# Kernel tuning notes

Hardware: AMD Instinct MI355X
Metric: run time of the kernel (lower is better)

## Reference

```python
import jax, jax.numpy as jnp
import numpy as np

S, O, H = 8, 1024, 1024
B, N = 32, 512

def setup_inputs() -> dict:
    key = jax.random.key(0)
    k1, k2, k3, k4 = jax.random.split(key, 4)
    x = jax.random.normal(k1, (B, N, H), dtype=jnp.float32)
    subject_id = jax.random.randint(k2, (B,), 0, S)
    # kaiming_uniform_(a=sqrt(5)) on [S,O,H]: fan_in=H, gain=sqrt(2/(1+5)), bound=gain*sqrt(3/fan_in)
    wbound = jnp.sqrt(2.0 / 6.0) * jnp.sqrt(3.0 / H)
    weight = jax.random.uniform(k3, (S, O, H), minval=-wbound, maxval=wbound, dtype=jnp.float32)
    bbound = 1.0 / jnp.sqrt(H)
    bias = jax.random.uniform(k4, (S, O), minval=-bbound, maxval=bbound, dtype=jnp.float32)
    return {"x": x, "subject_id": subject_id, "weight": weight, "bias": bias}

def reference(x, subject_id, weight, bias):
    # Per-sample weight gather + batched matmul + bias add
    W = weight[subject_id]          # [B, O, H]
    b = bias[subject_id]            # [B, O]
    y = jnp.einsum('bnh,boh->bno', x, W) + b[:, None, :]
    return y
```

## Files before the change

kernel.cpp:

```cpp
#include <hip/hip_runtime.h>


constexpr int S_DIM = 8;
constexpr int O_DIM = 1024;
constexpr int H_DIM = 1024;
constexpr int B_DIM = 32;
constexpr int N_DIM = 512;

constexpr int BM = 256;
constexpr int BN = 256;
constexpr int BK = 64;
constexpr int NKT = H_DIM / BK;

constexpr long long X_ELEMS = (long long)B_DIM * N_DIM * H_DIM;
constexpr size_t XB_BYTES = (size_t)X_ELEMS * 2;

typedef short bf16x8 __attribute__((ext_vector_type(8)));
typedef float f32x4 __attribute__((ext_vector_type(4)));
typedef float f32x2 __attribute__((ext_vector_type(2)));
typedef __bf16 bf16x2 __attribute__((ext_vector_type(2)));

__device__ __forceinline__ unsigned int cvt_pk_bf16(float a, float b) {
  f32x2 v;
  v[0] = a;
  v[1] = b;
  bf16x2 r = __builtin_convertvector(v, bf16x2);
  return __builtin_bit_cast(unsigned int, r);
}

__device__ __forceinline__ void gload_lds16(const void* g, void* l) {
  __builtin_amdgcn_global_load_lds(
      (const __attribute__((address_space(1))) unsigned int*)g,
      (__attribute__((address_space(3))) unsigned int*)l, 16, 0, 0);
}

__global__ __launch_bounds__(256) void cvt_kernel(
    const float* __restrict__ x, const float* __restrict__ w,
    unsigned short* __restrict__ xb, unsigned short* __restrict__ wb) {
  const int blk = blockIdx.x;
  const float* src;
  unsigned short* dst;
  long long base;
  if (blk < 4096) {
    src = x; dst = xb; base = (long long)blk * 4096;
  } else {
    src = w; dst = wb; base = (long long)(blk - 4096) * 4096;
  }
  const long long e0 = base + threadIdx.x * 4;
#pragma unroll
  for (int c = 0; c < 4; ++c) {
    const f32x4 v = __builtin_nontemporal_load((const f32x4*)(src + e0 + c * 1024));
    uint2 u;
    u.x = cvt_pk_bf16(v[0], v[1]);
    u.y = cvt_pk_bf16(v[2], v[3]);
    *(uint2*)(dst + e0 + c * 1024) = u;
  }
}

#define BAR() __builtin_amdgcn_s_barrier()
#define SB0() __builtin_amdgcn_sched_barrier(0)
#define VMW(N) asm volatile("s_waitcnt vmcnt(" #N ")" ::: "memory")
#define LGKM0()                                            \
  do {                                                     \
    asm volatile("s_waitcnt lgkmcnt(0)" ::: "memory");     \
    __builtin_amdgcn_sched_barrier(0);                     \
  } while (0)

#define LDA4T(DST, ABUF, MB)                                             \
  do {                                                                   \
    _Pragma("unroll") for (int m_ = 0; m_ < 4; ++m_) {                   \
      const int ar_ = wr * 128 + ((MB) + m_) * 16 + lcol;                \
      const unsigned short* ap_ = (ABUF) + ar_ * BK;                     \
      DST[m_][0] = *(const bf16x8*)(ap_ + (pc0 << 3));                   \
      DST[m_][1] = *(const bf16x8*)(ap_ + ((pc0 ^ 4) << 3));             \
    }                                                                    \
  } while (0)

#define LDB2T(DST, BBUF, NB)                                             \
  do {                                                                   \
    _Pragma("unroll") for (int n_ = 0; n_ < 2; ++n_) {                   \
      const int br_ = wc * 64 + ((NB) + n_) * 16 + lcol;                 \
      const unsigned short* bp_ = (BBUF) + br_ * BK;                     \
      DST[n_][0] = *(const bf16x8*)(bp_ + (pc0 << 3));                   \
      DST[n_][1] = *(const bf16x8*)(bp_ + ((pc0 ^ 4) << 3));             \
    }                                                                    \
  } while (0)

#define MM4(AF, BF, MB, NB)                                                 \
  do {                                                                      \
    _Pragma("unroll") for (int m_ = 0; m_ < 4; ++m_)                        \
    _Pragma("unroll") for (int n_ = 0; n_ < 2; ++n_)                        \
    _Pragma("unroll") for (int x_ = 0; x_ < 2; ++x_)                        \
      acc[(MB) + m_][(NB) + n_] = __builtin_amdgcn_mfma_f32_16x16x32_bf16(  \
          AF[m_][x_], BF[n_][x_], acc[(MB) + m_][(NB) + n_], 0, 0, 0);      \
  } while (0)

#define STAGE_A(H, DST, KT)                                                 \
  do {                                                                      \
    gload_lds16(agA + (size_t)((H) * 64) * H_DIM + (KT) * 64,               \
                (DST) + ((H) * 64 + wid * 8) * BK);                         \
    gload_lds16(agA + (size_t)((H) * 64 + 128) * H_DIM + (KT) * 64,         \
                (DST) + ((H) * 64 + 128 + wid * 8) * BK);                   \
  } while (0)

#define STAGE_B(S, DST, KT)                                                 \
  do {                                                                      \
    gload_lds16(bgB0 + (size_t)((S) * 32) * H_DIM + (KT) * 64,              \
                (DST) + (bq0 + (S) * 32) * BK);                             \
    gload_lds16(bgB1 + (size_t)((S) * 32) * H_DIM + (KT) * 64,              \
                (DST) + (bq1 + (S) * 32) * BK);                             \
  } while (0)

#define KTILE(KT, AC, BC, AO, BO)                                        \
  do {                                                                   \
        \
    LGKM0();                                                             \
    __builtin_amdgcn_s_setprio(1);                                       \
    MM4(af, bfL, 0, 0);                                                  \
    __builtin_amdgcn_s_setprio(0);                                       \
    LDB2T(bfH, BC, 2);                             \
    if ((KT) + 1 < NKT) STAGE_A(1, AO, (KT) + 1);                        \
    SB0();                                                               \
    BAR();                                                               \
                                                  \
    LGKM0();                                                             \
    __builtin_amdgcn_s_setprio(1);                                       \
    MM4(af, bfH, 0, 2);                                                  \
    __builtin_amdgcn_s_setprio(0);                                       \
    LDA4T(af, AC, 4);                           \
    if ((KT) + 1 < NKT) STAGE_B(1, BO, (KT) + 1);                        \
    SB0();                                                               \
    BAR();                                                               \
                                                  \
    LGKM0();                                                             \
    __builtin_amdgcn_s_setprio(1);                                       \
    MM4(af, bfH, 4, 2);                                                  \
    __builtin_amdgcn_s_setprio(0);                                       \
    if ((KT) + 2 < NKT) {                                                \
      STAGE_A(0, AC, (KT) + 2);                                          \
      STAGE_B(0, BC, (KT) + 2);                                          \
      VMW(8);            \
    } else if ((KT) + 2 == NKT) {                                        \
      VMW(4);                                                            \
    }                                                                    \
    SB0();                                                               \
    BAR();                                                               \
                                                  \
    LGKM0();                                                             \
    __builtin_amdgcn_s_setprio(1);                                       \
    MM4(af, bfL, 4, 0);                                                  \
    __builtin_amdgcn_s_setprio(0);                                       \
    if ((KT) + 1 < NKT) {                                                \
      LDA4T(af, AO, 0);                                 \
      LDB2T(bfL, BO, 0);                                \
      if ((KT) + 2 < NKT) VMW(4);          \
      else VMW(0);                   \
    }                                                                    \
    SB0();                                                               \
    BAR();                                                               \
  } while (0)

__global__ __launch_bounds__(512, 2) void scl_gemm(
    const unsigned short* __restrict__ xb, const int* __restrict__ subject_id,
    const unsigned short* __restrict__ wb, const float* __restrict__ bias,
    float* __restrict__ out) {
  __shared__ __align__(16) unsigned short As[2][BM * BK];
  __shared__ __align__(16) unsigned short Bs[2][BN * BK];

  const int tid = threadIdx.x;
  const int lane = tid & 63;
  const int wid = tid >> 6;
  const int wr = wid >> 2;
  const int wc = wid & 3;
  const int lcol = lane & 15;
  const int lq = lane >> 4;
  const int rl = lane >> 3;
  const int pc0 = lq ^ (lane & 7);

  const int bid = blockIdx.x;
  const int b = (bid & 7) * 4 + ((bid >> 3) & 3);
  const int t = bid >> 5;
  const int n0 = (t & 1) * BM;
  const int o0 = (t >> 1) * BN;
  const int sid = subject_id[b];

  const int skc = ((lane & 7) ^ rl) << 3;
  const unsigned short* agA =
      xb + (size_t)(b * N_DIM + n0 + wid * 8 + rl) * H_DIM + skc;
  const int bq0 = ((wid * 2) >> 2) * 64 + ((wid * 2) & 3) * 8;
  const int bq1 = ((wid * 2 + 1) >> 2) * 64 + ((wid * 2 + 1) & 3) * 8;
  const unsigned short* bgB0 =
      wb + (size_t)(sid * O_DIM + o0 + bq0 + rl) * H_DIM + skc;
  const unsigned short* bgB1 =
      wb + (size_t)(sid * O_DIM + o0 + bq1 + rl) * H_DIM + skc;

  unsigned short* const As0 = &As[0][0];
  unsigned short* const As1 = &As[1][0];
  unsigned short* const Bs0 = &Bs[0][0];
  unsigned short* const Bs1 = &Bs[1][0];

  f32x4 acc[8][4];
#pragma unroll
  for (int mi = 0; mi < 8; ++mi)
#pragma unroll
    for (int ni = 0; ni < 4; ++ni) {
      f32x4 z = {0.f, 0.f, 0.f, 0.f};
      acc[mi][ni] = z;
    }

  bf16x8 af[4][2];
  bf16x8 bfL[2][2];
  bf16x8 bfH[2][2];

  STAGE_A(0, As0, 0);
  STAGE_B(0, Bs0, 0);
  STAGE_A(1, As0, 0);
  STAGE_B(1, Bs0, 0);
  STAGE_A(0, As1, 1);
  STAGE_B(0, Bs1, 1);
  VMW(4);
  BAR();
  LDA4T(af, As0, 0);
  LDB2T(bfL, Bs0, 0);
  SB0();

#pragma unroll 1
  for (int kt = 0; kt < NKT; kt += 2) {
    KTILE(kt, As0, Bs0, As1, Bs1);
    KTILE(kt + 1, As1, Bs1, As0, Bs0);
  }

  float bv[4];
#pragma unroll
  for (int ni = 0; ni < 4; ++ni)
    bv[ni] = bias[sid * O_DIM + o0 + wc * 64 + ni * 16 + lcol];

  float* outb =
      out + (size_t)(b * N_DIM + n0 + wr * 128) * O_DIM + o0 + wc * 64 + lcol;
#pragma unroll
  for (int mi = 0; mi < 8; ++mi) {
#pragma unroll
    for (int r = 0; r < 4; ++r) {
      float* orow = outb + (size_t)(mi * 16 + lq * 4 + r) * O_DIM;
#pragma unroll
      for (int ni = 0; ni < 4; ++ni)
        orow[ni * 16] = acc[mi][ni][r] + bv[ni];
    }
  }
}

extern "C" void kernel_launch(void* const* d_in, const int* in_sizes, int n_in,
                              void* d_out, int out_size, void* d_ws, size_t ws_size,
                              hipStream_t stream) {
  const float* x = (const float*)d_in[0];
  const int* subject_id = (const int*)d_in[1];
  const float* weight = (const float*)d_in[2];
  const float* bias = (const float*)d_in[3];
  float* out = (float*)d_out;

  unsigned short* xb = (unsigned short*)d_ws;
  unsigned short* wb = (unsigned short*)((char*)d_ws + XB_BYTES);

  cvt_kernel<<<6144, 256, 0, stream>>>(x, weight, xb, wb);

  scl_gemm<<<256, 512, 0, stream>>>(xb, subject_id, wb, bias, out);
}
```

Before: 177.6 us.

## Fuse fp32-to-bf16 conversion of x into GEMM LDS path with triple buffering

Removes the separate conversion pass over x: the GEMM now stages fp32 x tiles directly into LDS and converts them to bf16 while loading MFMA fragments. Only the weights still go through a standalone conversion kernel. To make room for fp32 A tiles, BK drops to 32 and the pipeline becomes a three-stage LDS ring with new swizzles and a two-phase k-tile schedule. This avoids writing and rereading a 32 MB bf16 copy of x, but it doubles A-side LDS traffic per element, adds conversion ALU work in the inner loop, and halves work per barrier.

```diff
diff --git a/kernel.cpp b/kernel.cpp
--- a/kernel.cpp
+++ b/kernel.cpp
@@ -9,16 +9,14 @@
 
 constexpr int BM = 256;
 constexpr int BN = 256;
-constexpr int BK = 64;
+constexpr int BK = 32;
 constexpr int NKT = H_DIM / BK;
-
-constexpr long long X_ELEMS = (long long)B_DIM * N_DIM * H_DIM;
-constexpr size_t XB_BYTES = (size_t)X_ELEMS * 2;
 
 typedef short bf16x8 __attribute__((ext_vector_type(8)));
 typedef float f32x4 __attribute__((ext_vector_type(4)));
 typedef float f32x2 __attribute__((ext_vector_type(2)));
 typedef __bf16 bf16x2 __attribute__((ext_vector_type(2)));
+typedef unsigned int u32x4 __attribute__((ext_vector_type(4)));
 
 __device__ __forceinline__ unsigned int cvt_pk_bf16(float a, float b) {
   f32x2 v;
@@ -34,26 +32,16 @@
       (__attribute__((address_space(3))) unsigned int*)l, 16, 0, 0);
 }
 
-__global__ __launch_bounds__(256) void cvt_kernel(
-    const float* __restrict__ x, const float* __restrict__ w,
-    unsigned short* __restrict__ xb, unsigned short* __restrict__ wb) {
-  const int blk = blockIdx.x;
-  const float* src;
-  unsigned short* dst;
-  long long base;
-  if (blk < 4096) {
-    src = x; dst = xb; base = (long long)blk * 4096;
-  } else {
-    src = w; dst = wb; base = (long long)(blk - 4096) * 4096;
-  }
-  const long long e0 = base + threadIdx.x * 4;
+__global__ __launch_bounds__(256) void cvt_w(const float* __restrict__ w,
+                                             unsigned short* __restrict__ wb) {
+  const long long e0 = (long long)blockIdx.x * 4096 + threadIdx.x * 4;
 #pragma unroll
   for (int c = 0; c < 4; ++c) {
-    const f32x4 v = __builtin_nontemporal_load((const f32x4*)(src + e0 + c * 1024));
+    const f32x4 v = __builtin_nontemporal_load((const f32x4*)(w + e0 + c * 1024));
     uint2 u;
     u.x = cvt_pk_bf16(v[0], v[1]);
     u.y = cvt_pk_bf16(v[2], v[3]);
-    *(uint2*)(dst + e0 + c * 1024) = u;
+    *(uint2*)(wb + e0 + c * 1024) = u;
   }
 }
 
@@ -66,106 +54,89 @@
     __builtin_amdgcn_sched_barrier(0);                     \
   } while (0)
 
-#define LDA4T(DST, ABUF, MB)                                             \
+#define LDAF(DST, ABUF, MB)                                              \
   do {                                                                   \
     _Pragma("unroll") for (int m_ = 0; m_ < 4; ++m_) {                   \
       const int ar_ = wr * 128 + ((MB) + m_) * 16 + lcol;                \
-      const unsigned short* ap_ = (ABUF) + ar_ * BK;                     \
-      DST[m_][0] = *(const bf16x8*)(ap_ + (pc0 << 3));                   \
-      DST[m_][1] = *(const bf16x8*)(ap_ + ((pc0 ^ 4) << 3));             \
-    }                                                                    \
-  } while (0)
-
-#define LDB2T(DST, BBUF, NB)                                             \
-  do {                                                                   \
-    _Pragma("unroll") for (int n_ = 0; n_ < 2; ++n_) {                   \
-      const int br_ = wc * 64 + ((NB) + n_) * 16 + lcol;                 \
-      const unsigned short* bp_ = (BBUF) + br_ * BK;                     \
-      DST[n_][0] = *(const bf16x8*)(bp_ + (pc0 << 3));                   \
-      DST[n_][1] = *(const bf16x8*)(bp_ + ((pc0 ^ 4) << 3));             \
-    }                                                                    \
-  } while (0)
-
-#define MM4(AF, BF, MB, NB)                                                 \
-  do {                                                                      \
-    _Pragma("unroll") for (int m_ = 0; m_ < 4; ++m_)                        \
-    _Pragma("unroll") for (int n_ = 0; n_ < 2; ++n_)                        \
-    _Pragma("unroll") for (int x_ = 0; x_ < 2; ++x_)                        \
-      acc[(MB) + m_][(NB) + n_] = __builtin_amdgcn_mfma_f32_16x16x32_bf16(  \
-          AF[m_][x_], BF[n_][x_], acc[(MB) + m_][(NB) + n_], 0, 0, 0);      \
-  } while (0)
-
-#define STAGE_A(H, DST, KT)                                                 \
-  do {                                                                      \
-    gload_lds16(agA + (size_t)((H) * 64) * H_DIM + (KT) * 64,               \
-                (DST) + ((H) * 64 + wid * 8) * BK);                         \
-    gload_lds16(agA + (size_t)((H) * 64 + 128) * H_DIM + (KT) * 64,         \
-                (DST) + ((H) * 64 + 128 + wid * 8) * BK);                   \
-  } while (0)
-
-#define STAGE_B(S, DST, KT)                                                 \
-  do {                                                                      \
-    gload_lds16(bgB0 + (size_t)((S) * 32) * H_DIM + (KT) * 64,              \
-                (DST) + (bq0 + (S) * 32) * BK);                             \
-    gload_lds16(bgB1 + (size_t)((S) * 32) * H_DIM + (KT) * 64,              \
-                (DST) + (bq1 + (S) * 32) * BK);                             \
-  } while (0)
-
-#define KTILE(KT, AC, BC, AO, BO)                                        \
-  do {                                                                   \
-        \
+      const float* ap_ = (ABUF) + ar_ * 32;                              \
+      const f32x4 lo_ = *(const f32x4*)(ap_ + pA0);                      \
+      const f32x4 hi_ = *(const f32x4*)(ap_ + pA1);                      \
+      u32x4 t_;                                                          \
+      t_[0] = cvt_pk_bf16(lo_[0], lo_[1]);                               \
+      t_[1] = cvt_pk_bf16(lo_[2], lo_[3]);                               \
+      t_[2] = cvt_pk_bf16(hi_[0], hi_[1]);                               \
+      t_[3] = cvt_pk_bf16(hi_[2], hi_[3]);                               \
+      DST[m_] = __builtin_bit_cast(bf16x8, t_);                          \
+    }                                                                    \
+  } while (0)
+
+#define LDBF(DST, BBUF)                                                  \
+  do {                                                                   \
+    _Pragma("unroll") for (int n_ = 0; n_ < 4; ++n_) {                   \
+      const int br_ = wc * 64 + n_ * 16 + lcol;                          \
+      DST[n_] = *(const bf16x8*)((BBUF) + br_ * 32 + pB);                \
+    }                                                                    \
+  } while (0)
+
+#define MMQ(AF, MB)                                                      \
+  do {                                                                   \
+    _Pragma("unroll") for (int m_ = 0; m_ < 4; ++m_)                     \
+    _Pragma("unroll") for (int n_ = 0; n_ < 4; ++n_)                     \
+      acc[(MB) + m_][n_] = __builtin_amdgcn_mfma_f32_16x16x32_bf16(      \
+          AF[m_], bf[n_], acc[(MB) + m_][n_], 0, 0, 0);                  \
+  } while (0)
+
+#define STAGE_AU(I, DSTA, KT)                                            \
+  gload_lds16(agA + (size_t)(I) * 8 * H_DIM + (size_t)(KT) * 32,         \
+              (DSTA) + (wid * 32 + (I) * 8) * 32)
+#define STAGE_BU(J, DSTB, KT)                                            \
+  gload_lds16(bgB + (size_t)(J) * 16 * H_DIM + (size_t)(KT) * 32,        \
+              (DSTB) + (wid * 32 + (J) * 16) * 32)
+#define STAGE6(AS, BS, KT)                                               \
+  do {                                                                   \
+    STAGE_AU(0, AS, KT);                                                 \
+    STAGE_AU(1, AS, KT);                                                 \
+    STAGE_AU(2, AS, KT);                                                 \
+    STAGE_AU(3, AS, KT);                                                 \
+    STAGE_BU(0, BS, KT);                                                 \
+    STAGE_BU(1, BS, KT);                                                 \
+  } while (0)
+
+#define KTILE(KT, AC, BC, AN, BN, AS, BS)                                \
+  do {                                                                   \
+             \
     LGKM0();                                                             \
     __builtin_amdgcn_s_setprio(1);                                       \
-    MM4(af, bfL, 0, 0);                                                  \
+    MMQ(afL, 0);                                                         \
     __builtin_amdgcn_s_setprio(0);                                       \
-    LDB2T(bfH, BC, 2);                             \
-    if ((KT) + 1 < NKT) STAGE_A(1, AO, (KT) + 1);                        \
+    if ((KT) + 2 < NKT) {                                                \
+      STAGE6(AS, BS, (KT) + 2);                                          \
+      VMW(6);              \
+    } else if ((KT) + 1 < NKT) {                                         \
+      VMW(0);     \
+    }                                                                    \
+    LDAF(afH, AC, 4);                                                    \
     SB0();                                                               \
     BAR();                                                               \
-                                                  \
+                                                         \
     LGKM0();                                                             \
     __builtin_amdgcn_s_setprio(1);                                       \
-    MM4(af, bfH, 0, 2);                                                  \
+    MMQ(afH, 4);                                                         \
     __builtin_amdgcn_s_setprio(0);                                       \
-    LDA4T(af, AC, 4);                           \
-    if ((KT) + 1 < NKT) STAGE_B(1, BO, (KT) + 1);                        \
+    if ((KT) + 1 < NKT) {                                                \
+      LDAF(afL, AN, 0);      \
+      LDBF(bf, BN);                                                      \
+    }                                                                    \
     SB0();                                                               \
     BAR();                                                               \
-                                                  \
-    LGKM0();                                                             \
-    __builtin_amdgcn_s_setprio(1);                                       \
-    MM4(af, bfH, 4, 2);                                                  \
-    __builtin_amdgcn_s_setprio(0);                                       \
-    if ((KT) + 2 < NKT) {                                                \
-      STAGE_A(0, AC, (KT) + 2);                                          \
-      STAGE_B(0, BC, (KT) + 2);                                          \
-      VMW(8);            \
-    } else if ((KT) + 2 == NKT) {                                        \
-      VMW(4);                                                            \
-    }                                                                    \
-    SB0();                                                               \
-    BAR();                                                               \
-                                                  \
-    LGKM0();                                                             \
-    __builtin_amdgcn_s_setprio(1);                                       \
-    MM4(af, bfL, 4, 0);                                                  \
-    __builtin_amdgcn_s_setprio(0);                                       \
-    if ((KT) + 1 < NKT) {                                                \
-      LDA4T(af, AO, 0);                                 \
-      LDB2T(bfL, BO, 0);                                \
-      if ((KT) + 2 < NKT) VMW(4);          \
-      else VMW(0);                   \
-    }                                                                    \
-    SB0();                                                               \
-    BAR();                                                               \
   } while (0)
 
 __global__ __launch_bounds__(512, 2) void scl_gemm(
-    const unsigned short* __restrict__ xb, const int* __restrict__ subject_id,
+    const float* __restrict__ xg, const int* __restrict__ subject_id,
     const unsigned short* __restrict__ wb, const float* __restrict__ bias,
     float* __restrict__ out) {
-  __shared__ __align__(16) unsigned short As[2][BM * BK];
-  __shared__ __align__(16) unsigned short Bs[2][BN * BK];
+  __shared__ __align__(16) float Afs[3][BM * 32];
+  __shared__ __align__(16) unsigned short Bbs[3][BN * 32];
 
   const int tid = threadIdx.x;
   const int lane = tid & 63;
@@ -174,8 +145,10 @@
   const int wc = wid & 3;
   const int lcol = lane & 15;
   const int lq = lane >> 4;
-  const int rl = lane >> 3;
-  const int pc0 = lq ^ (lane & 7);
+
+  const int pA0 = (((2 * lq) ^ (lcol & 7)) << 2);
+  const int pA1 = (((2 * lq + 1) ^ (lcol & 7)) << 2);
+  const int pB = ((lq ^ (lcol & 3) ^ ((lcol >> 2) & 3)) << 3);
 
   const int bid = blockIdx.x;
   const int b = (bid & 7) * 4 + ((bid >> 3) & 3);
@@ -184,20 +157,21 @@
   const int o0 = (t >> 1) * BN;
   const int sid = subject_id[b];
 
-  const int skc = ((lane & 7) ^ rl) << 3;
-  const unsigned short* agA =
-      xb + (size_t)(b * N_DIM + n0 + wid * 8 + rl) * H_DIM + skc;
-  const int bq0 = ((wid * 2) >> 2) * 64 + ((wid * 2) & 3) * 8;
-  const int bq1 = ((wid * 2 + 1) >> 2) * 64 + ((wid * 2 + 1) & 3) * 8;
-  const unsigned short* bgB0 =
-      wb + (size_t)(sid * O_DIM + o0 + bq0 + rl) * H_DIM + skc;
-  const unsigned short* bgB1 =
-      wb + (size_t)(sid * O_DIM + o0 + bq1 + rl) * H_DIM + skc;
-
-  unsigned short* const As0 = &As[0][0];
-  unsigned short* const As1 = &As[1][0];
-  unsigned short* const Bs0 = &Bs[0][0];
-  unsigned short* const Bs1 = &Bs[1][0];
+  const int rlA = lane >> 3;
+  const int skcA = ((lane & 7) ^ rlA) << 2;
+  const float* agA =
+      xg + (size_t)(b * N_DIM + n0 + wid * 32 + rlA) * H_DIM + skcA;
+  const int skcB =
+      (((lane & 3) ^ ((lane >> 2) & 3) ^ ((lane >> 4) & 3))) << 3;
+  const unsigned short* bgB =
+      wb + (size_t)(sid * O_DIM + o0 + wid * 32 + (lane >> 2)) * H_DIM + skcB;
+
+  float* const Af0 = &Afs[0][0];
+  float* const Af1 = &Afs[1][0];
+  float* const Af2 = &Afs[2][0];
+  unsigned short* const Bb0 = &Bbs[0][0];
+  unsigned short* const Bb1 = &Bbs[1][0];
+  unsigned short* const Bb2 = &Bbs[2][0];
 
   f32x4 acc[8][4];
 #pragma unroll
@@ -208,27 +182,26 @@
       acc[mi][ni] = z;
     }
 
-  bf16x8 af[4][2];
-  bf16x8 bfL[2][2];
-  bf16x8 bfH[2][2];
-
-  STAGE_A(0, As0, 0);
-  STAGE_B(0, Bs0, 0);
-  STAGE_A(1, As0, 0);
-  STAGE_B(1, Bs0, 0);
-  STAGE_A(0, As1, 1);
-  STAGE_B(0, Bs1, 1);
-  VMW(4);
+  bf16x8 afL[4];
+  bf16x8 afH[4];
+  bf16x8 bf[4];
+
+  STAGE6(Af0, Bb0, 0);
+  STAGE6(Af1, Bb1, 1);
+  VMW(6);
   BAR();
-  LDA4T(af, As0, 0);
-  LDB2T(bfL, Bs0, 0);
+  LDAF(afL, Af0, 0);
+  LDBF(bf, Bb0);
   SB0();
 
 #pragma unroll 1
-  for (int kt = 0; kt < NKT; kt += 2) {
-    KTILE(kt, As0, Bs0, As1, Bs1);
-    KTILE(kt + 1, As1, Bs1, As0, Bs0);
+  for (int kt0 = 0; kt0 < 30; kt0 += 3) {
+    KTILE(kt0,     Af0, Bb0, Af1, Bb1, Af2, Bb2);
+    KTILE(kt0 + 1, Af1, Bb1, Af2, Bb2, Af0, Bb0);
+    KTILE(kt0 + 2, Af2, Bb2, Af0, Bb0, Af1, Bb1);
   }
+  KTILE(30, Af0, Bb0, Af1, Bb1, Af2, Bb2);
+  KTILE(31, Af1, Bb1, Af2, Bb2, Af0, Bb0);
 
   float bv[4];
 #pragma unroll
@@ -258,10 +231,9 @@
   const float* bias = (const float*)d_in[3];
   float* out = (float*)d_out;
 
-  unsigned short* xb = (unsigned short*)d_ws;
-  unsigned short* wb = (unsigned short*)((char*)d_ws + XB_BYTES);
-
-  cvt_kernel<<<6144, 256, 0, stream>>>(x, weight, xb, wb);
-
-  scl_gemm<<<256, 512, 0, stream>>>(xb, subject_id, wb, bias, out);
-}
+  unsigned short* wb = (unsigned short*)d_ws;
+
+  cvt_w<<<2048, 256, 0, stream>>>(weight, wb);
+
+  scl_gemm<<<256, 512, 0, stream>>>(x, subject_id, wb, bias, out);
+}
```

Measured after the change: 199.5 us. +12.3%, slower.

## Fuse fp32-to-bf16 conversion into GEMM tile loads, drop separate convert kernel

Applied to the files above, without the earlier changes.

Removes the standalone conversion kernel that wrote bf16 copies of x and weight to workspace. The GEMM now loads fp32 tiles from global memory into registers, converts them to bf16 and writes them into swizzled LDS, instead of using direct global-to-LDS loads of pre-converted data. This avoids a full extra read/write pass over x and the weights, but doubles the global bytes per tile, adds register pressure, and forces vmcnt(0) waits inside the loop, which reduce load/compute overlap.

```diff
diff --git a/kernel.cpp b/kernel.cpp
--- a/kernel.cpp
+++ b/kernel.cpp
@@ -12,13 +12,11 @@
 constexpr int BK = 64;
 constexpr int NKT = H_DIM / BK;
 
-constexpr long long X_ELEMS = (long long)B_DIM * N_DIM * H_DIM;
-constexpr size_t XB_BYTES = (size_t)X_ELEMS * 2;
-
 typedef short bf16x8 __attribute__((ext_vector_type(8)));
 typedef float f32x4 __attribute__((ext_vector_type(4)));
 typedef float f32x2 __attribute__((ext_vector_type(2)));
 typedef __bf16 bf16x2 __attribute__((ext_vector_type(2)));
+typedef unsigned int u32x4 __attribute__((ext_vector_type(4)));
 
 __device__ __forceinline__ unsigned int cvt_pk_bf16(float a, float b) {
   f32x2 v;
@@ -28,38 +26,10 @@
   return __builtin_bit_cast(unsigned int, r);
 }
 
-__device__ __forceinline__ void gload_lds16(const void* g, void* l) {
-  __builtin_amdgcn_global_load_lds(
-      (const __attribute__((address_space(1))) unsigned int*)g,
-      (__attribute__((address_space(3))) unsigned int*)l, 16, 0, 0);
-}
-
-__global__ __launch_bounds__(256) void cvt_kernel(
-    const float* __restrict__ x, const float* __restrict__ w,
-    unsigned short* __restrict__ xb, unsigned short* __restrict__ wb) {
-  const int blk = blockIdx.x;
-  const float* src;
-  unsigned short* dst;
-  long long base;
-  if (blk < 4096) {
-    src = x; dst = xb; base = (long long)blk * 4096;
-  } else {
-    src = w; dst = wb; base = (long long)(blk - 4096) * 4096;
-  }
-  const long long e0 = base + threadIdx.x * 4;
-#pragma unroll
-  for (int c = 0; c < 4; ++c) {
-    const f32x4 v = __builtin_nontemporal_load((const f32x4*)(src + e0 + c * 1024));
-    uint2 u;
-    u.x = cvt_pk_bf16(v[0], v[1]);
-    u.y = cvt_pk_bf16(v[2], v[3]);
-    *(uint2*)(dst + e0 + c * 1024) = u;
-  }
-}
-
 #define BAR() __builtin_amdgcn_s_barrier()
 #define SB0() __builtin_amdgcn_sched_barrier(0)
 #define VMW(N) asm volatile("s_waitcnt vmcnt(" #N ")" ::: "memory")
+#define LGKMW(N) asm volatile("s_waitcnt lgkmcnt(" #N ")" ::: "memory")
 #define LGKM0()                                            \
   do {                                                     \
     asm volatile("s_waitcnt lgkmcnt(0)" ::: "memory");     \
@@ -95,20 +65,34 @@
           AF[m_][x_], BF[n_][x_], acc[(MB) + m_][(NB) + n_], 0, 0, 0);      \
   } while (0)
 
-#define STAGE_A(H, DST, KT)                                                 \
-  do {                                                                      \
-    gload_lds16(agA + (size_t)((H) * 64) * H_DIM + (KT) * 64,               \
-                (DST) + ((H) * 64 + wid * 8) * BK);                         \
-    gload_lds16(agA + (size_t)((H) * 64 + 128) * H_DIM + (KT) * 64,         \
-                (DST) + ((H) * 64 + 128 + wid * 8) * BK);                   \
-  } while (0)
-
-#define STAGE_B(S, DST, KT)                                                 \
-  do {                                                                      \
-    gload_lds16(bgB0 + (size_t)((S) * 32) * H_DIM + (KT) * 64,              \
-                (DST) + (bq0 + (S) * 32) * BK);                             \
-    gload_lds16(bgB1 + (size_t)((S) * 32) * H_DIM + (KT) * 64,              \
-                (DST) + (bq1 + (S) * 32) * BK);                             \
+#define GLOADA(KT)                                                         \
+  do {                                                                     \
+    _Pragma("unroll") for (int i_ = 0; i_ < 4; ++i_) {                     \
+      const float* p_ = agA + (size_t)i_ * 8 * H_DIM + (size_t)(KT) * 64;  \
+      ga[i_][0] = *(const f32x4*)p_;                                       \
+      ga[i_][1] = *(const f32x4*)(p_ + 4);                                 \
+    }                                                                      \
+  } while (0)
+
+#define GLOADB(KT)                                                         \
+  do {                                                                     \
+    _Pragma("unroll") for (int i_ = 0; i_ < 4; ++i_) {                     \
+      const float* p_ = bgB + (size_t)i_ * 8 * H_DIM + (size_t)(KT) * 64;  \
+      gb[i_][0] = *(const f32x4*)p_;                                       \
+      gb[i_][1] = *(const f32x4*)(p_ + 4);                                 \
+    }                                                                      \
+  } while (0)
+
+#define DSWR(SRC, DST)                                                     \
+  do {                                                                     \
+    _Pragma("unroll") for (int i_ = 0; i_ < 4; ++i_) {                     \
+      u32x4 t_;                                                            \
+      t_[0] = cvt_pk_bf16(SRC[i_][0][0], SRC[i_][0][1]);                   \
+      t_[1] = cvt_pk_bf16(SRC[i_][0][2], SRC[i_][0][3]);                   \
+      t_[2] = cvt_pk_bf16(SRC[i_][1][0], SRC[i_][1][1]);                   \
+      t_[3] = cvt_pk_bf16(SRC[i_][1][2], SRC[i_][1][3]);                   \
+      *(u32x4*)((DST) + swoff + i_ * 8 * BK) = t_;                         \
+    }                                                                      \
   } while (0)
 
 #define KTILE(KT, AC, BC, AO, BO)                                        \
@@ -118,8 +102,8 @@
     __builtin_amdgcn_s_setprio(1);                                       \
     MM4(af, bfL, 0, 0);                                                  \
     __builtin_amdgcn_s_setprio(0);                                       \
+    if ((KT) + 1 < NKT) GLOADA((KT) + 1);                                \
     LDB2T(bfH, BC, 2);                             \
-    if ((KT) + 1 < NKT) STAGE_A(1, AO, (KT) + 1);                        \
     SB0();                                                               \
     BAR();                                                               \
                                                   \
@@ -127,8 +111,14 @@
     __builtin_amdgcn_s_setprio(1);                                       \
     MM4(af, bfH, 0, 2);                                                  \
     __builtin_amdgcn_s_setprio(0);                                       \
+    if ((KT) + 1 < NKT) {                                                \
+      VMW(0);                   \
+      DSWR(ga, AO);                                                      \
+      SB0();                 \
+      GLOADB((KT) + 1);                                                  \
+    }                                                                    \
     LDA4T(af, AC, 4);                           \
-    if ((KT) + 1 < NKT) STAGE_B(1, BO, (KT) + 1);                        \
+    LGKMW(8);                  \
     SB0();                                                               \
     BAR();                                                               \
                                                   \
@@ -136,12 +126,10 @@
     __builtin_amdgcn_s_setprio(1);                                       \
     MM4(af, bfH, 4, 2);                                                  \
     __builtin_amdgcn_s_setprio(0);                                       \
-    if ((KT) + 2 < NKT) {                                                \
-      STAGE_A(0, AC, (KT) + 2);                                          \
-      STAGE_B(0, BC, (KT) + 2);                                          \
-      VMW(8);            \
-    } else if ((KT) + 2 == NKT) {                                        \
-      VMW(4);                                                            \
+    if ((KT) + 1 < NKT) {                                                \
+      VMW(0);                                        \
+      DSWR(gb, BO);                                                      \
+      LGKMW(0);                         \
     }                                                                    \
     SB0();                                                               \
     BAR();                                                               \
@@ -153,16 +141,14 @@
     if ((KT) + 1 < NKT) {                                                \
       LDA4T(af, AO, 0);                                 \
       LDB2T(bfL, BO, 0);                                \
-      if ((KT) + 2 < NKT) VMW(4);          \
-      else VMW(0);                   \
     }                                                                    \
     SB0();                                                               \
     BAR();                                                               \
   } while (0)
 
 __global__ __launch_bounds__(512, 2) void scl_gemm(
-    const unsigned short* __restrict__ xb, const int* __restrict__ subject_id,
-    const unsigned short* __restrict__ wb, const float* __restrict__ bias,
+    const float* __restrict__ xg, const int* __restrict__ subject_id,
+    const float* __restrict__ wg, const float* __restrict__ bias,
     float* __restrict__ out) {
   __shared__ __align__(16) unsigned short As[2][BM * BK];
   __shared__ __align__(16) unsigned short Bs[2][BN * BK];
@@ -185,14 +171,11 @@
   const int sid = subject_id[b];
 
   const int skc = ((lane & 7) ^ rl) << 3;
-  const unsigned short* agA =
-      xb + (size_t)(b * N_DIM + n0 + wid * 8 + rl) * H_DIM + skc;
-  const int bq0 = ((wid * 2) >> 2) * 64 + ((wid * 2) & 3) * 8;
-  const int bq1 = ((wid * 2 + 1) >> 2) * 64 + ((wid * 2 + 1) & 3) * 8;
-  const unsigned short* bgB0 =
-      wb + (size_t)(sid * O_DIM + o0 + bq0 + rl) * H_DIM + skc;
-  const unsigned short* bgB1 =
-      wb + (size_t)(sid * O_DIM + o0 + bq1 + rl) * H_DIM + skc;
+  const float* agA =
+      xg + (size_t)(b * N_DIM + n0 + wid * 32 + rl) * H_DIM + skc;
+  const float* bgB =
+      wg + (size_t)(sid * O_DIM + o0 + wid * 32 + rl) * H_DIM + skc;
+  const int swoff = (wid * 32 + rl) * BK + (lane & 7) * 8;
 
   unsigned short* const As0 = &As[0][0];
   unsigned short* const As1 = &As[1][0];
@@ -211,14 +194,16 @@
   bf16x8 af[4][2];
   bf16x8 bfL[2][2];
   bf16x8 bfH[2][2];
-
-  STAGE_A(0, As0, 0);
-  STAGE_B(0, Bs0, 0);
-  STAGE_A(1, As0, 0);
-  STAGE_B(1, Bs0, 0);
-  STAGE_A(0, As1, 1);
-  STAGE_B(0, Bs1, 1);
-  VMW(4);
+  f32x4 ga[4][2];
+  f32x4 gb[4][2];
+
+  GLOADA(0);
+  VMW(0);
+  DSWR(ga, As0);
+  GLOADB(0);
+  VMW(0);
+  DSWR(gb, Bs0);
+  LGKMW(0);
   BAR();
   LDA4T(af, As0, 0);
   LDB2T(bfL, Bs0, 0);
@@ -258,10 +243,5 @@
   const float* bias = (const float*)d_in[3];
   float* out = (float*)d_out;
 
-  unsigned short* xb = (unsigned short*)d_ws;
-  unsigned short* wb = (unsigned short*)((char*)d_ws + XB_BYTES);
-
-  cvt_kernel<<<6144, 256, 0, stream>>>(x, weight, xb, wb);
-
-  scl_gemm<<<256, 512, 0, stream>>>(xb, subject_id, wb, bias, out);
+  scl_gemm<<<256, 512, 0, stream>>>(x, subject_id, weight, bias, out);
 }
```

Result: slower. 259.3 us (+46.0%).
